# Performance work log

Measured on AMD Instinct MI355X. Metric: run time of the kernel, lower is better.

## Reference

```python
import jax, jax.numpy as jnp
import numpy as np

B, H, W, C = 2, 96, 96, 96
GROUPS = 32
EPS = 1e-5


def group_norm_dim1(x, gamma, beta):
    # Faithful to torch nn.GroupNorm(32, C) applied to an NHWC tensor:
    # dim 1 (H) is treated as the channel axis, normalized over (H//G, W, C) per group.
    b, h, w, c = x.shape
    xg = x.reshape(b, GROUPS, h // GROUPS, w, c)
    mean = xg.mean(axis=(2, 3, 4), keepdims=True)
    var = xg.var(axis=(2, 3, 4), keepdims=True)
    xn = ((xg - mean) * jax.lax.rsqrt(var + EPS)).reshape(b, h, w, c)
    return xn * gamma[None, :, None, None] + beta[None, :, None, None]


def setup_inputs() -> dict:
    key = jax.random.key(0)
    ks = jax.random.split(key, 9)
    s = 1.0 / np.sqrt(C)  # kaiming-uniform-ish scale
    x = jax.random.normal(ks[0], (B, H, W, C), dtype=jnp.float32)
    Wq = jax.random.uniform(ks[1], (C, C), jnp.float32, -s, s)
    Wk = jax.random.uniform(ks[2], (C, C), jnp.float32, -s, s)
    Wv = jax.random.uniform(ks[3], (C, C), jnp.float32, -s, s)
    Wp = jax.random.uniform(ks[4], (C, C), jnp.float32, -s, s)
    return {
        "x": x,
        "gamma": jnp.ones((H,), jnp.float32),   # GroupNorm affine weight (over dim 1)
        "beta": jnp.zeros((H,), jnp.float32),
        "Wq": Wq, "bq": jnp.zeros((C,), jnp.float32),
        "Wk": Wk, "bk": jnp.zeros((C,), jnp.float32),
        "Wv": Wv, "bv": jnp.zeros((C,), jnp.float32),
        "Wp": Wp, "bp": jnp.zeros((C,), jnp.float32),
    }


def reference(x, gamma, beta, Wq, bq, Wk, bk, Wv, bv, Wp, bp):
    b, h, w, c = x.shape
    hn = group_norm_dim1(x, gamma, beta)
    q = hn @ Wq + bq  # [B,H,W,C], Nin = contract last dim
    k = hn @ Wk + bk
    v = hn @ Wv + bv
    scale = c ** (-0.5)
    # full dense spatial attention: [B, HW, HW]
    scores = jnp.einsum('bxyc,buvc->bxyuv', q, k) * scale
    attn = jax.nn.softmax(scores.reshape(b, h, w, h * w), axis=-1).reshape(b, h, w, h, w)
    o = jnp.einsum('bxyuv,buvc->bxyc', attn, v)
    return x + (o @ Wp + bp)
```

## Files before the change

kernel.cpp:

```cpp
#include <hip/hip_runtime.h>
#include <hip/hip_bf16.h>
#include <stdint.h>

#define B_   2
#define H_   96
#define W_   96
#define C_   96
#define HW_  (H_ * W_)
#define NT_  (B_ * HW_)
#define EPS_ 1e-5f
#define KSPLIT  8
#define KRANGE  (HW_ / KSPLIT)
#define ATT_NIT (KRANGE / 32)
#define SCL (0.10206207261596575f * 1.4426950408889634f)

typedef __hip_bfloat16 bf16;
typedef __attribute__((ext_vector_type(8))) short short8;
typedef __attribute__((ext_vector_type(16))) float f32x16;

__device__ __forceinline__ uint32_t pk_bf16(float a, float b) {
    uint32_t ua = __float_as_uint(a) + 0x8000u;
    uint32_t ub = __float_as_uint(b) + 0x8000u;
    return __builtin_amdgcn_perm(ub, ua, 0x07060302u);
}
__device__ __forceinline__ float bl(uint32_t u) { uint32_t x = u << 16;         return *(float*)&x; }
__device__ __forceinline__ float bh(uint32_t u) { uint32_t x = u & 0xffff0000u; return *(float*)&x; }
__device__ __forceinline__ float fexp2(float x) { return __builtin_amdgcn_exp2f(x); }
__device__ __forceinline__ short8 lds_frag(const short* p) {
    union { int2 h[2]; short8 v; } t;
    t.h[0] = *(const int2*)(p);
    t.h[1] = *(const int2*)(p + 4);
    return t.v;
}

__device__ __forceinline__ void load_hn_frags(
        const float* __restrict__ x, const float2* __restrict__ stats,
        const float* __restrict__ gamma, const float* __restrict__ beta,
        int token, int hh, short8* hf) {
    int b = token / HW_;
    int h = (token % HW_) / W_;
    float2 st = stats[b * 32 + h / 3];
    float g0 = gamma[h];
    float ga = g0 * st.y;
    float be = beta[h] - st.x * st.y * g0;
    const float* xr = x + (size_t)token * C_ + hh * 8;
    #pragma unroll
    for (int s = 0; s < 6; ++s) {
        float4 a = *(const float4*)(xr + s * 16);
        float4 c = *(const float4*)(xr + s * 16 + 4);
        union { uint32_t w[4]; short8 v; } f;
        f.w[0] = pk_bf16(a.x * ga + be, a.y * ga + be);
        f.w[1] = pk_bf16(a.z * ga + be, a.w * ga + be);
        f.w[2] = pk_bf16(c.x * ga + be, c.y * ga + be);
        f.w[3] = pk_bf16(c.z * ga + be, c.w * ga + be);
        hf[s] = f.v;
    }
}

__global__ __launch_bounds__(1024)
void stats_prep_kernel(const float* __restrict__ x, float2* __restrict__ stats,
                       const float* __restrict__ Wq, const float* __restrict__ Wk,
                       const float* __restrict__ Wv, const float* __restrict__ Wp,
                       bf16* __restrict__ wqt, bf16* __restrict__ wkt,
                       bf16* __restrict__ wvt, bf16* __restrict__ wpt) {
    int blk = blockIdx.x;
    int tid = threadIdx.x;
    if (blk >= 64) {
        int wsel = blk - 64;
        const float* S = (wsel == 0) ? Wq : (wsel == 1) ? Wk : (wsel == 2) ? Wv : Wp;
        bf16* D = (wsel == 0) ? wqt : (wsel == 1) ? wkt : (wsel == 2) ? wvt : wpt;
        for (int i = tid; i < C_ * C_; i += 1024) {
            int r = i / C_, c = i % C_;
            D[c * C_ + r] = __float2bfloat16(S[r * C_ + c]);
        }
        return;
    }
    int b = blk >> 5, g = blk & 31;
    const int n = 3 * W_ * C_;
    size_t base = (size_t)(b * H_ + 3 * g) * (W_ * C_);
    float s = 0.f, ss = 0.f;
    for (int i = tid; i < n; i += 1024) {
        float v = x[base + i];
        s += v; ss += v * v;
    }
    __shared__ float rs[1024], rss[1024];
    rs[tid] = s; rss[tid] = ss;
    __syncthreads();
    for (int off = 512; off > 0; off >>= 1) {
        if (tid < off) { rs[tid] += rs[tid + off]; rss[tid] += rss[tid + off]; }
        __syncthreads();
    }
    if (tid == 0) {
        float mean = rs[0] / n;
        float var  = rss[0] / n - mean * mean;
        stats[blk] = make_float2(mean, rsqrtf(var + EPS_));
    }
}

__global__ __launch_bounds__(256)
void qkv_kernel(const float* __restrict__ x, const float2* __restrict__ stats,
                const float* __restrict__ gamma, const float* __restrict__ beta,
                const bf16* __restrict__ wqt, const bf16* __restrict__ wkt,
                const bf16* __restrict__ wvt,
                const float* __restrict__ bq, const float* __restrict__ bk,
                const float* __restrict__ bv,
                bf16* __restrict__ qb, bf16* __restrict__ kb, bf16* __restrict__ vt) {
    int blk = blockIdx.x;
    int w = blk / 144, grp = blk % 144;
    int wave = threadIdx.x >> 6, lane = threadIdx.x & 63;
    int tile = grp * 4 + wave;
    int n0 = tile * 32;
    int col = lane & 31, hh = lane >> 5;
    int token = n0 + col;

    short8 hf[6];
    load_hn_frags(x, stats, gamma, beta, token, hh, hf);

    if (w == 2) {
        int bb = n0 / HW_, nl0 = n0 % HW_;
        #pragma unroll
        for (int t = 0; t < 3; ++t) {
            int c = t * 32 + col;
            const bf16* wrow = wvt + (size_t)c * C_ + hh * 8;
            f32x16 acc = (f32x16)(0.f);
            #pragma unroll
            for (int s = 0; s < 6; ++s)
                acc = __builtin_amdgcn_mfma_f32_32x32x16_bf16(
                        hf[s], *(const short8*)(wrow + s * 16), acc, 0, 0, 0);
            float bias = bv[c];
            bf16* dst = vt + ((size_t)bb * C_ + c) * HW_ + nl0 + 4 * hh;
            #pragma unroll
            for (int g = 0; g < 4; ++g) {
                uint2 pk = make_uint2(pk_bf16(acc[4 * g] + bias, acc[4 * g + 1] + bias),
                                      pk_bf16(acc[4 * g + 2] + bias, acc[4 * g + 3] + bias));
                *(uint2*)(dst + 8 * g) = pk;
            }
        }
    } else {
        const bf16*  wt   = (w == 0) ? wqt : wkt;
        const float* bias = (w == 0) ? bq : bk;
        bf16*        dst  = (w == 0) ? qb : kb;
        float        scl  = (w == 0) ? SCL : 1.f;
        #pragma unroll
        for (int t = 0; t < 3; ++t) {
            const bf16* wrow = wt + (size_t)(t * 32 + col) * C_ + hh * 8;
            f32x16 acc = (f32x16)(0.f);
            #pragma unroll
            for (int s = 0; s < 6; ++s)
                acc = __builtin_amdgcn_mfma_f32_32x32x16_bf16(
                        *(const short8*)(wrow + s * 16), hf[s], acc, 0, 0, 0);
            #pragma unroll
            for (int g = 0; g < 4; ++g) {
                int nb = t * 32 + 8 * g + 4 * hh;
                float4 b4 = *(const float4*)(bias + nb);
                float v0 = (acc[4 * g]     + b4.x) * scl;
                float v1 = (acc[4 * g + 1] + b4.y) * scl;
                float v2 = (acc[4 * g + 2] + b4.z) * scl;
                float v3 = (acc[4 * g + 3] + b4.w) * scl;
                uint2 pk = make_uint2(pk_bf16(v0, v1), pk_bf16(v2, v3));
                *(uint2*)(dst + (size_t)token * C_ + nb) = pk;
            }
        }
    }
}

__global__ __launch_bounds__(256, 3)
void attn_kernel(const bf16* __restrict__ qb, const bf16* __restrict__ kb,
                 const bf16* __restrict__ vt,
                 bf16* __restrict__ pob, float* __restrict__ pl) {
    __shared__ short Kbuf[2][32 * 100];
    __shared__ short Vbuf[2][96 * 36];

    int blk = blockIdx.x;
    int ks = blk & 7, qg = blk >> 3;
    int b = qg / 72, g72 = qg % 72;
    int n0 = g72 * 128;
    int tid = threadIdx.x;
    int wave = tid >> 6, lane = tid & 63;
    int col = lane & 31, hh = lane >> 5;

    const bf16* kbb = kb + ((size_t)b * HW_ + (size_t)ks * KRANGE) * C_;
    const bf16* vbb = vt + (size_t)b * C_ * HW_ + (size_t)ks * KRANGE;

    int n = n0 + wave * 32 + col;
    short8 qf[6];
    {
        const bf16* qrow = qb + (size_t)(b * HW_ + n) * C_ + hh * 8;
        #pragma unroll
        for (int s = 0; s < 6; ++s) qf[s] = *(const short8*)(qrow + s * 16);
    }

    f32x16 oa[3];
    #pragma unroll
    for (int t = 0; t < 3; ++t) oa[t] = (f32x16)(0.f);
    float l_run = 0.f;

    bool isK = (tid < 128);
    int t128 = tid & 127;
    int ldsA[3], ldsB[3], goff[3];
    #pragma unroll
    for (int j = 0; j < 3; ++j) {
        int c = t128 + 128 * j;
        if (isK) {
            ldsA[j] = (c / 12) * 100 + (c % 12) * 8;
            ldsB[j] = ldsA[j] + 4;
            goff[j] = c * 8;
        } else {
            int rw = c >> 2, g = c & 3;
            ldsA[j] = rw * 36 + (2 * g - (g & 1)) * 4;
            ldsB[j] = rw * 36 + (2 * g + 2 - (g & 1)) * 4;
            goff[j] = rw * HW_ + g * 8;
        }
    }
    const bf16* gbase = isK ? kbb : vbb;
    const int itstep = isK ? (32 * C_) : 32;

    {
        short* sb = isK ? Kbuf[0] : Vbuf[0];
        #pragma unroll
        for (int j = 0; j < 3; ++j) {
            int4 r = *(const int4*)(gbase + goff[j]);
            *(int2*)(sb + ldsA[j]) = make_int2(r.x, r.y);
            *(int2*)(sb + ldsB[j]) = make_int2(r.z, r.w);
        }
    }
    __syncthreads();

    union FU { uint32_t w[4]; short8 v; };

    for (int it = 0; it < ATT_NIT; ++it) {
        int cur = it & 1;
        bool pre = (it + 1 < ATT_NIT);
        int4 r0, r1, r2;
        if (pre) {
            const bf16* g = gbase + (size_t)(it + 1) * itstep;
            r0 = *(const int4*)(g + goff[0]);
            r1 = *(const int4*)(g + goff[1]);
            r2 = *(const int4*)(g + goff[2]);
        }

        const short* Kc = Kbuf[cur];
        const short* Vc = Vbuf[cur];

        short8 kf[6];
        #pragma unroll
        for (int s = 0; s < 6; ++s)
            kf[s] = lds_frag(Kc + col * 100 + s * 16 + hh * 8);

        f32x16 st = (f32x16)(0.f);
        #pragma unroll
        for (int s = 0; s < 6; ++s)
            st = __builtin_amdgcn_mfma_f32_32x32x16_bf16(kf[s], qf[s], st, 0, 0, 0);

        float p[16], ls = 0.f;
        #pragma unroll
        for (int i = 0; i < 16; ++i) { p[i] = fexp2(st[i]); ls += p[i]; }
        l_run += ls;
        FU f0, f1;
        #pragma unroll
        for (int j = 0; j < 4; ++j) {
            f0.w[j] = pk_bf16(p[2 * j],     p[2 * j + 1]);
            f1.w[j] = pk_bf16(p[8 + 2 * j], p[8 + 2 * j + 1]);
        }

        #pragma unroll
        for (int t = 0; t < 3; ++t) {
            const short* vr = Vc + (32 * t + col) * 36 + hh * 8;
            short8 vf0 = lds_frag(vr);
            short8 vf1 = lds_frag(vr + 16);
            oa[t] = __builtin_amdgcn_mfma_f32_32x32x16_bf16(vf0, f0.v, oa[t], 0, 0, 0);
            oa[t] = __builtin_amdgcn_mfma_f32_32x32x16_bf16(vf1, f1.v, oa[t], 0, 0, 0);
        }

        if (pre) {
            short* sb = isK ? Kbuf[cur ^ 1] : Vbuf[cur ^ 1];
            *(int2*)(sb + ldsA[0]) = make_int2(r0.x, r0.y);
            *(int2*)(sb + ldsB[0]) = make_int2(r0.z, r0.w);
            *(int2*)(sb + ldsA[1]) = make_int2(r1.x, r1.y);
            *(int2*)(sb + ldsB[1]) = make_int2(r1.z, r1.w);
            *(int2*)(sb + ldsA[2]) = make_int2(r2.x, r2.y);
            *(int2*)(sb + ldsB[2]) = make_int2(r2.z, r2.w);
        }
        __syncthreads();
    }

    {
        size_t bq = (size_t)b * HW_ + n;
        float lt = l_run + __shfl_xor(l_run, 32, 64);
        if (hh == 0) pl[(size_t)ks * NT_ + bq] = lt;
        #pragma unroll
        for (int t = 0; t < 3; ++t)
            #pragma unroll
            for (int g = 0; g < 4; ++g) {
                int c0 = t * 32 + 8 * g + 4 * hh;
                uint2 pk = make_uint2(
                    pk_bf16(oa[t][4 * g],     oa[t][4 * g + 1]),
                    pk_bf16(oa[t][4 * g + 2], oa[t][4 * g + 3]));
                *(uint2*)(pob + ((size_t)ks * NT_ + bq) * C_ + c0) = pk;
            }
    }
}

__global__ __launch_bounds__(256)
void out_kernel(const float* __restrict__ x,
                const bf16* __restrict__ pob, const float* __restrict__ pl,
                const bf16* __restrict__ wpt, const float* __restrict__ bp,
                float* __restrict__ out) {
    int wave = threadIdx.x >> 6, lane = threadIdx.x & 63;
    int tile = blockIdx.x * 4 + wave;
    int n0 = tile * 32;
    int col = lane & 31, hh = lane >> 5;
    int token = n0 + col;

    float l = 0.f;
    #pragma unroll
    for (int ksp = 0; ksp < KSPLIT; ++ksp) l += pl[(size_t)ksp * NT_ + token];
    float inv = 1.f / l;

    short8 of[6];
    #pragma unroll
    for (int s = 0; s < 6; ++s) {
        float acc[8] = {0.f};
        #pragma unroll
        for (int ksp = 0; ksp < KSPLIT; ++ksp) {
            uint4 u = *(const uint4*)(pob + ((size_t)ksp * NT_ + token) * C_ + s * 16 + hh * 8);
            acc[0] += bl(u.x); acc[1] += bh(u.x);
            acc[2] += bl(u.y); acc[3] += bh(u.y);
            acc[4] += bl(u.z); acc[5] += bh(u.z);
            acc[6] += bl(u.w); acc[7] += bh(u.w);
        }
        union { uint32_t w[4]; short8 v; } f;
        #pragma unroll
        for (int j = 0; j < 4; ++j)
            f.w[j] = pk_bf16(acc[2 * j] * inv, acc[2 * j + 1] * inv);
        of[s] = f.v;
    }

    #pragma unroll
    for (int t = 0; t < 3; ++t) {
        f32x16 acc = (f32x16)(0.f);
        const bf16* wrow = wpt + (size_t)(t * 32 + col) * C_ + hh * 8;
        #pragma unroll
        for (int s = 0; s < 6; ++s)
            acc = __builtin_amdgcn_mfma_f32_32x32x16_bf16(
                    *(const short8*)(wrow + s * 16), of[s], acc, 0, 0, 0);
        #pragma unroll
        for (int g = 0; g < 4; ++g) {
            int nb = t * 32 + 8 * g + 4 * hh;
            float4 b4 = *(const float4*)(bp + nb);
            float4 xv = *(const float4*)(x + (size_t)token * C_ + nb);
            float4 rr;
            rr.x = xv.x + acc[4 * g]     + b4.x;
            rr.y = xv.y + acc[4 * g + 1] + b4.y;
            rr.z = xv.z + acc[4 * g + 2] + b4.z;
            rr.w = xv.w + acc[4 * g + 3] + b4.w;
            *(float4*)(out + (size_t)token * C_ + nb) = rr;
        }
    }
}

extern "C" void kernel_launch(void* const* d_in, const int* in_sizes, int n_in,
                              void* d_out, int out_size, void* d_ws, size_t ws_size,
                              hipStream_t stream) {
    const float* x     = (const float*)d_in[0];
    const float* gamma = (const float*)d_in[1];
    const float* beta  = (const float*)d_in[2];
    const float* Wq    = (const float*)d_in[3];
    const float* bq    = (const float*)d_in[4];
    const float* Wk    = (const float*)d_in[5];
    const float* bk    = (const float*)d_in[6];
    const float* Wv    = (const float*)d_in[7];
    const float* bv    = (const float*)d_in[8];
    const float* Wp    = (const float*)d_in[9];
    const float* bp    = (const float*)d_in[10];
    float* out = (float*)d_out;

    char* ws = (char*)d_ws;
    const size_t TB = (size_t)NT_ * C_ * 2;
    bf16* qb  = (bf16*)(ws);
    bf16* kb  = (bf16*)(ws + TB);
    bf16* vt  = (bf16*)(ws + 2 * TB);
    bf16* wqt = (bf16*)(ws + 3 * TB);
    bf16* wkt = (bf16*)(ws + 3 * TB + 18432);
    bf16* wvt = (bf16*)(ws + 3 * TB + 2 * 18432);
    bf16* wpt = (bf16*)(ws + 3 * TB + 3 * 18432);
    float2* stats = (float2*)(ws + 3 * TB + 4 * 18432);
    bf16*  pob = (bf16*)(ws + 3 * TB + 4 * 18432 + 512);
    float* pl  = (float*)(ws + 3 * TB + 4 * 18432 + 512
                          + (size_t)KSPLIT * NT_ * C_ * 2);

    hipLaunchKernelGGL(stats_prep_kernel, dim3(68), dim3(1024), 0, stream,
                       x, stats, Wq, Wk, Wv, Wp, wqt, wkt, wvt, wpt);
    hipLaunchKernelGGL(qkv_kernel, dim3(3 * 144), dim3(256), 0, stream,
                       x, stats, gamma, beta, wqt, wkt, wvt, bq, bk, bv, qb, kb, vt);
    hipLaunchKernelGGL(attn_kernel, dim3(1152), dim3(256), 0, stream,
                       qb, kb, vt, pob, pl);
    hipLaunchKernelGGL(out_kernel, dim3(144), dim3(256), 0, stream,
                       x, pob, pl, wpt, bp, out);
}
```

Before: 200.7 us.

## Vectorize stats reduction, raise attention occupancy, spread output projection across more blocks

The group-norm stats loop now reads float4 and reduces with wave shuffles instead of a 1024-entry shared-memory tree. The attention kernel's launch bounds ask for 4 blocks per CU instead of 3, which may force register spills. The output kernel now gives each block one 32-token tile: all threads cooperatively sum the split-K partials into LDS, then three waves each compute one 32-column slice of the projection. The grid grows from 144 to 576 blocks for better CU coverage, at the cost of an extra LDS round trip and a quarter of the threads idling during the MFMA phase.

```diff
diff --git a/kernel.cpp b/kernel.cpp
--- a/kernel.cpp
+++ b/kernel.cpp
@@ -76,23 +76,30 @@
         return;
     }
     int b = blk >> 5, g = blk & 31;
-    const int n = 3 * W_ * C_;
-    size_t base = (size_t)(b * H_ + 3 * g) * (W_ * C_);
+    const int n4 = 3 * W_ * C_ / 4;
+    const float4* xb = (const float4*)(x + (size_t)(b * H_ + 3 * g) * (W_ * C_));
     float s = 0.f, ss = 0.f;
-    for (int i = tid; i < n; i += 1024) {
-        float v = x[base + i];
-        s += v; ss += v * v;
-    }
-    __shared__ float rs[1024], rss[1024];
-    rs[tid] = s; rss[tid] = ss;
+    for (int i = tid; i < n4; i += 1024) {
+        float4 v = xb[i];
+        s  += v.x + v.y + v.z + v.w;
+        ss += v.x * v.x + v.y * v.y + v.z * v.z + v.w * v.w;
+    }
+    #pragma unroll
+    for (int off = 1; off < 64; off <<= 1) {
+        s  += __shfl_xor(s, off, 64);
+        ss += __shfl_xor(ss, off, 64);
+    }
+    __shared__ float rs[16], rss[16];
+    int wid = tid >> 6;
+    if ((tid & 63) == 0) { rs[wid] = s; rss[wid] = ss; }
     __syncthreads();
-    for (int off = 512; off > 0; off >>= 1) {
-        if (tid < off) { rs[tid] += rs[tid + off]; rss[tid] += rss[tid + off]; }
-        __syncthreads();
-    }
     if (tid == 0) {
-        float mean = rs[0] / n;
-        float var  = rss[0] / n - mean * mean;
+        float ts = 0.f, tss = 0.f;
+        #pragma unroll
+        for (int i = 0; i < 16; ++i) { ts += rs[i]; tss += rss[i]; }
+        const float n = 3 * W_ * C_;
+        float mean = ts / n;
+        float var  = tss / n - mean * mean;
         stats[blk] = make_float2(mean, rsqrtf(var + EPS_));
     }
 }
@@ -164,7 +171,7 @@
     }
 }
 
-__global__ __launch_bounds__(256, 3)
+__global__ __launch_bounds__(256, 4)
 void attn_kernel(const bf16* __restrict__ qb, const bf16* __restrict__ kb,
                  const bf16* __restrict__ vt,
                  bf16* __restrict__ pob, float* __restrict__ pl) {
@@ -306,56 +313,70 @@
                 const bf16* __restrict__ pob, const float* __restrict__ pl,
                 const bf16* __restrict__ wpt, const float* __restrict__ bp,
                 float* __restrict__ out) {
-    int wave = threadIdx.x >> 6, lane = threadIdx.x & 63;
-    int tile = blockIdx.x * 4 + wave;
+    __shared__ short ofs[32 * 100];
+    __shared__ float linv_s[32];
+
+    int tile = blockIdx.x;
     int n0 = tile * 32;
-    int col = lane & 31, hh = lane >> 5;
-    int token = n0 + col;
-
-    float l = 0.f;
-    #pragma unroll
-    for (int ksp = 0; ksp < KSPLIT; ++ksp) l += pl[(size_t)ksp * NT_ + token];
-    float inv = 1.f / l;
-
-    short8 of[6];
-    #pragma unroll
-    for (int s = 0; s < 6; ++s) {
-        float acc[8] = {0.f};
+    int tid = threadIdx.x;
+
+    if (tid < 32) {
+        int token = n0 + tid;
+        float l = 0.f;
+        #pragma unroll
+        for (int ksp = 0; ksp < KSPLIT; ++ksp) l += pl[(size_t)ksp * NT_ + token];
+        linv_s[tid] = 1.f / l;
+    }
+    __syncthreads();
+
+    for (int pos = tid; pos < 384; pos += 256) {
+        int token = pos / 12, c8 = (pos % 12) * 8;
+        float acc[8] = {0.f, 0.f, 0.f, 0.f, 0.f, 0.f, 0.f, 0.f};
         #pragma unroll
         for (int ksp = 0; ksp < KSPLIT; ++ksp) {
-            uint4 u = *(const uint4*)(pob + ((size_t)ksp * NT_ + token) * C_ + s * 16 + hh * 8);
+            uint4 u = *(const uint4*)(pob + ((size_t)ksp * NT_ + n0 + token) * C_ + c8);
             acc[0] += bl(u.x); acc[1] += bh(u.x);
             acc[2] += bl(u.y); acc[3] += bh(u.y);
             acc[4] += bl(u.z); acc[5] += bh(u.z);
             acc[6] += bl(u.w); acc[7] += bh(u.w);
         }
-        union { uint32_t w[4]; short8 v; } f;
-        #pragma unroll
-        for (int j = 0; j < 4; ++j)
-            f.w[j] = pk_bf16(acc[2 * j] * inv, acc[2 * j + 1] * inv);
-        of[s] = f.v;
-    }
-
-    #pragma unroll
-    for (int t = 0; t < 3; ++t) {
-        f32x16 acc = (f32x16)(0.f);
-        const bf16* wrow = wpt + (size_t)(t * 32 + col) * C_ + hh * 8;
-        #pragma unroll
-        for (int s = 0; s < 6; ++s)
-            acc = __builtin_amdgcn_mfma_f32_32x32x16_bf16(
-                    *(const short8*)(wrow + s * 16), of[s], acc, 0, 0, 0);
-        #pragma unroll
-        for (int g = 0; g < 4; ++g) {
-            int nb = t * 32 + 8 * g + 4 * hh;
-            float4 b4 = *(const float4*)(bp + nb);
-            float4 xv = *(const float4*)(x + (size_t)token * C_ + nb);
-            float4 rr;
-            rr.x = xv.x + acc[4 * g]     + b4.x;
-            rr.y = xv.y + acc[4 * g + 1] + b4.y;
-            rr.z = xv.z + acc[4 * g + 2] + b4.z;
-            rr.w = xv.w + acc[4 * g + 3] + b4.w;
-            *(float4*)(out + (size_t)token * C_ + nb) = rr;
-        }
+        float inv = linv_s[token];
+        short* dst = ofs + token * 100 + c8;
+        *(int2*)(dst)     = make_int2(pk_bf16(acc[0] * inv, acc[1] * inv),
+                                      pk_bf16(acc[2] * inv, acc[3] * inv));
+        *(int2*)(dst + 4) = make_int2(pk_bf16(acc[4] * inv, acc[5] * inv),
+                                      pk_bf16(acc[6] * inv, acc[7] * inv));
+    }
+    __syncthreads();
+
+    int wave = tid >> 6;
+    if (wave >= 3) return;
+    int lane = tid & 63, col = lane & 31, hh = lane >> 5;
+    int t = wave;
+    int token = n0 + col;
+
+    short8 of[6];
+    #pragma unroll
+    for (int s = 0; s < 6; ++s)
+        of[s] = lds_frag(ofs + col * 100 + s * 16 + hh * 8);
+
+    f32x16 acc = (f32x16)(0.f);
+    const bf16* wrow = wpt + (size_t)(t * 32 + col) * C_ + hh * 8;
+    #pragma unroll
+    for (int s = 0; s < 6; ++s)
+        acc = __builtin_amdgcn_mfma_f32_32x32x16_bf16(
+                *(const short8*)(wrow + s * 16), of[s], acc, 0, 0, 0);
+    #pragma unroll
+    for (int g = 0; g < 4; ++g) {
+        int nb = t * 32 + 8 * g + 4 * hh;
+        float4 b4 = *(const float4*)(bp + nb);
+        float4 xv = *(const float4*)(x + (size_t)token * C_ + nb);
+        float4 rr;
+        rr.x = xv.x + acc[4 * g]     + b4.x;
+        rr.y = xv.y + acc[4 * g + 1] + b4.y;
+        rr.z = xv.z + acc[4 * g + 2] + b4.z;
+        rr.w = xv.w + acc[4 * g + 3] + b4.w;
+        *(float4*)(out + (size_t)token * C_ + nb) = rr;
     }
 }
 
@@ -395,6 +416,6 @@
                        x, stats, gamma, beta, wqt, wkt, wvt, bq, bk, bv, qb, kb, vt);
     hipLaunchKernelGGL(attn_kernel, dim3(1152), dim3(256), 0, stream,
                        qb, kb, vt, pob, pl);
-    hipLaunchKernelGGL(out_kernel, dim3(144), dim3(256), 0, stream,
+    hipLaunchKernelGGL(out_kernel, dim3(576), dim3(256), 0, stream,
                        x, pob, pl, wpt, bp, out);
 }
```

New measurement: 193.5 us. -3.6%, faster.
